# Performance work log

Measured on AMD Instinct MI355X. Metric: run time of the kernel, lower is better.

Reference implementation:

```python
import jax, jax.numpy as jnp
import numpy as np

HEADS = 64
DIM_HEAD = 64
SCALE = DIM_HEAD ** -0.5
EPS = 1e-6


def setup_inputs() -> dict:
    key = jax.random.key(0)
    ks = jax.random.split(key, 6)
    b, s, dim = 2, 4096, 1024
    inner = HEADS * DIM_HEAD  # 4096
    std = 0.02
    return {
        "x": jax.random.normal(ks[0], (b, s, dim), dtype=jnp.float32),
        "Wq": jax.random.normal(ks[1], (dim, inner), dtype=jnp.float32) * std,
        "Wk": jax.random.normal(ks[2], (dim, inner), dtype=jnp.float32) * std,
        "Wv": jax.random.normal(ks[3], (dim, inner), dtype=jnp.float32) * std,
        "Wo": jax.random.normal(ks[4], (inner, dim), dtype=jnp.float32) * std,
        "bo": jnp.zeros((dim,), dtype=jnp.float32),
    }


def reference(x, Wq, Wk, Wv, Wo, bo):
    b, s, dim = x.shape
    h, dh = HEADS, DIM_HEAD
    # projections -> [b, s, h, dh]
    q = (x @ Wq).reshape(b, s, h, dh)
    k = (x @ Wk).reshape(b, s, h, dh)
    v = (x @ Wv).reshape(b, s, h, dh)
    # kernel feature map (relu) + scale on q
    q = jax.nn.relu(q) * SCALE
    k = jax.nn.relu(k)
    # NOTE: faithful to the source, these einsums contract over the HEAD axis
    # per token (i, j index heads; d indexes dim_head).
    kv = jnp.einsum('bsid,bsjd->bsdj', k, v)          # [b, s, dh, h]
    out = jnp.einsum('bsid,bsdj->bsij', q, kv)        # [b, s, h, h]
    q_norm = jnp.einsum('bsid,bsd->bsi', q, k.sum(axis=2))  # [b, s, h]
    out = out / (q_norm[..., None] + EPS)
    out = out.reshape(b, s, h * h)                    # h*h == h*dh since h == dh
    return out @ Wo + bo
```

## Files before the change

### kernel.cpp

```cpp
#include <hip/hip_runtime.h>
#include <hip/hip_bf16.h>
#include <cstdint>

#define M_TOK 8192
#define DIM   1024
#define INNER 4096
#define HEADS 64
#define DH    64
#define QSCALE 0.125f
#define EPS    1e-6f

typedef __hip_bfloat16 bf16;
typedef __bf16 bf16x8_t __attribute__((ext_vector_type(8)));
typedef float f32x4_t __attribute__((ext_vector_type(4)));

__device__ __forceinline__ float bfbits2f(unsigned short u) {
  return __uint_as_float(((unsigned)u) << 16);
}
__device__ __forceinline__ unsigned short f2bfbits(float f) {
  __hip_bfloat16 h = __float2bfloat16(f);
  unsigned short u;
  __builtin_memcpy(&u, &h, 2);
  return u;
}

__device__ __forceinline__ void load_lds16(const void* g, void* l) {
  __builtin_amdgcn_global_load_lds(
      (__attribute__((address_space(1))) void*)g,
      (__attribute__((address_space(3))) void*)l, 16, 0, 0);
}

__device__ __forceinline__ void asm_barrier() {
  asm volatile("s_barrier" ::: "memory");
}

#define LGKM_SB(N) do { \
    asm volatile("s_waitcnt lgkmcnt(" #N ")" ::: "memory"); \
    __builtin_amdgcn_sched_barrier(0); } while (0)

__device__ __forceinline__ void swizzle_xy(int& bx, int& by) {
  const int gx = gridDim.x, gy = gridDim.y;
  const int id  = blockIdx.x + gx * blockIdx.y;
  const int per = gy >> 3;
  const int xcd = id & 7;
  const int s   = id >> 3;
  by = xcd * per + (s % per);
  bx = s / per;
}

__global__ __launch_bounds__(256) void prep_kernel(
    const float* __restrict__ x, unsigned short* __restrict__ xb,
    const float* __restrict__ Wk, const float* __restrict__ Wv,
    unsigned short* __restrict__ WtKV)
{
  const int bid = blockIdx.x;
  if (bid < 8192) {
    const int i = bid * 256 + threadIdx.x;
    const float4 v = reinterpret_cast<const float4*>(x)[i];
    ushort4 o;
    o.x = f2bfbits(v.x); o.y = f2bfbits(v.y);
    o.z = f2bfbits(v.z); o.w = f2bfbits(v.w);
    reinterpret_cast<ushort4*>(xb)[i] = o;
    return;
  }
  __shared__ float tile[32][33];
  const int t    = bid - 8192;
  const int z    = t >> 12;
  const int tt   = t & 4095;
  const float* W = z ? Wv : Wk;
  unsigned short* dst = WtKV + (size_t)z * DIM * INNER;
  const int bx = (tt & 127) * 32;
  const int by = (tt >> 7) * 32;
  const int tx = threadIdx.x & 31;
  const int ty = threadIdx.x >> 5;
#pragma unroll
  for (int k = 0; k < 4; ++k)
    tile[ty + k * 8][tx] = W[(size_t)(by + ty + k * 8) * INNER + bx + tx];
  __syncthreads();
#pragma unroll
  for (int k = 0; k < 4; ++k)
    dst[(size_t)(bx + ty + k * 8) * DIM + by + tx] = f2bfbits(tile[tx][ty + k * 8]);
}

__global__ __launch_bounds__(256) void tcast_kernel(
    const float* __restrict__ W, unsigned short* __restrict__ Wt, int R, int C)
{
  __shared__ float tile[32][33];
  const int bx = blockIdx.x * 32;
  const int by = blockIdx.y * 32;
  const int tx = threadIdx.x & 31;
  const int ty = threadIdx.x >> 5;
#pragma unroll
  for (int k = 0; k < 4; ++k)
    tile[ty + k * 8][tx] = W[(size_t)(by + ty + k * 8) * C + bx + tx];
  __syncthreads();
#pragma unroll
  for (int k = 0; k < 4; ++k)
    Wt[(size_t)(bx + ty + k * 8) * R + by + tx] = f2bfbits(tile[tx][ty + k * 8]);
}

__device__ __forceinline__ void stage_half(
    const unsigned short* __restrict__ G, unsigned short* L,
    int rowbase, int k0, int K, int h, int tid)
{
#pragma unroll
  for (int j = 0; j < 2; ++j) {
    const int q  = h * 1024 + j * 512 + tid;
    const int r  = q >> 3;
    const int cg = (tid & 7) ^ (r & 7);
    load_lds16(&G[(size_t)(rowbase + r) * K + k0 + cg * 8], &L[q * 8]);
  }
}

__device__ __forceinline__ void read_af4(
    const unsigned short* __restrict__ Ac, bf16x8_t (&af)[8][2],
    int m0, int wm, int l15, int quad)
{
#pragma unroll
  for (int mt = 0; mt < 4; ++mt) {
    const int r = wm + (m0 + mt) * 16 + l15;
#pragma unroll
    for (int kt = 0; kt < 2; ++kt) {
      const int s = (kt * 4 + quad) ^ (r & 7);
      af[m0 + mt][kt] = *reinterpret_cast<const bf16x8_t*>(&Ac[r * 64 + s * 8]);
    }
  }
}

__device__ __forceinline__ void read_bf2(
    const unsigned short* __restrict__ Bc, bf16x8_t (&bfr)[4][2],
    int n0, int wn, int l15, int quad)
{
#pragma unroll
  for (int nt = 0; nt < 2; ++nt) {
    const int r = wn + (n0 + nt) * 16 + l15;
#pragma unroll
    for (int kt = 0; kt < 2; ++kt) {
      const int s = (kt * 4 + quad) ^ (r & 7);
      bfr[n0 + nt][kt] = *reinterpret_cast<const bf16x8_t*>(&Bc[r * 64 + s * 8]);
    }
  }
}

__device__ __forceinline__ void mfma_quad(
    f32x4_t (&acc)[8][4], const bf16x8_t (&af)[8][2],
    const bf16x8_t (&bfr)[4][2], int m0, int n0)
{
  __builtin_amdgcn_s_setprio(1);
#pragma unroll
  for (int mt = m0; mt < m0 + 4; ++mt)
#pragma unroll
    for (int nt = n0; nt < n0 + 2; ++nt) {
      acc[mt][nt] = __builtin_amdgcn_mfma_f32_16x16x32_bf16(
          af[mt][0], bfr[nt][0], acc[mt][nt], 0, 0, 0);
      acc[mt][nt] = __builtin_amdgcn_mfma_f32_16x16x32_bf16(
          af[mt][1], bfr[nt][1], acc[mt][nt], 0, 0, 0);
    }
  __builtin_amdgcn_s_setprio(0);
}

template <int MODE, int DUAL>
__global__ __launch_bounds__(512, 2) void gemm256(
    const unsigned short* __restrict__ A,
    const unsigned short* __restrict__ Bt,
    unsigned short* __restrict__ C0,
    unsigned short* __restrict__ C1,
    int N, int K)
{
  __shared__ __align__(16) unsigned short As[2][256 * 64];
  __shared__ __align__(16) unsigned short Bs[2][256 * 64];

  int bxi, byi;
  swizzle_xy(bxi, byi);
  const int tid  = threadIdx.x;
  const int bm   = byi * 256;
  const int bn   = bxi * 256;
  const int lane = tid & 63;
  const int w    = tid >> 6;
  const int wm   = (w >> 2) * 128;
  const int wn   = (w & 3) * 64;
  const int quad = lane >> 4;
  const int l15  = lane & 15;

  f32x4_t acc[8][4];
#pragma unroll
  for (int mt = 0; mt < 8; ++mt)
#pragma unroll
    for (int nt = 0; nt < 4; ++nt) acc[mt][nt] = (f32x4_t){0.f, 0.f, 0.f, 0.f};

  const int NT = K >> 6;

  bf16x8_t af[8][2], bfr[4][2];

  stage_half(A,  As[0], bm, 0,  K, 0, tid);
  stage_half(A,  As[0], bm, 0,  K, 1, tid);
  stage_half(Bt, Bs[0], bn, 0,  K, 0, tid);
  stage_half(Bt, Bs[0], bn, 0,  K, 1, tid);
  stage_half(A,  As[1], bm, 64, K, 0, tid);
  stage_half(A,  As[1], bm, 64, K, 1, tid);
  asm volatile("s_waitcnt vmcnt(4)" ::: "memory");
  asm_barrier();
  __builtin_amdgcn_sched_barrier(0);
  read_af4(As[0], af, 0, wm, l15, quad);
  read_bf2(Bs[0], bfr, 0, wn, l15, quad);

  for (int T = 0; T < NT; ++T) {
    const int c = T & 1;
    const unsigned short* Ac = As[c];
    const unsigned short* Bc = Bs[c];
    unsigned short* Bnx = Bs[c ^ 1];
    unsigned short* Anx = As[c];
    const int kB = (T + 1) * 64;
    const int kA = (T + 2) * 64;
    const bool pB = (T + 1 < NT);
    const bool pA = (T + 2 < NT);

    read_af4(Ac, af, 4, wm, l15, quad);
    LGKM_SB(8);
    mfma_quad(acc, af, bfr, 0, 0);

    read_bf2(Bc, bfr, 2, wn, l15, quad);
    if (pB) stage_half(Bt, Bnx, bn, kB, K, 0, tid);
    LGKM_SB(4);
    mfma_quad(acc, af, bfr, 4, 0);

    if (pB) stage_half(Bt, Bnx, bn, kB, K, 1, tid);
    if (pA) stage_half(A, Anx, bm, kA, K, 0, tid);
    LGKM_SB(0);
    mfma_quad(acc, af, bfr, 0, 2);

    if (pA) stage_half(A, Anx, bm, kA, K, 1, tid);
    mfma_quad(acc, af, bfr, 4, 2);
    if (T < NT - 2) {
      asm volatile("s_waitcnt vmcnt(4)" ::: "memory");
    } else {
      asm volatile("s_waitcnt vmcnt(0)" ::: "memory");
    }
    asm_barrier();
    __builtin_amdgcn_sched_barrier(0);
    if (T + 1 < NT) {
      read_af4(As[c ^ 1], af, 0, wm, l15, quad);
      read_bf2(Bs[c ^ 1], bfr, 0, wn, l15, quad);
    }
  }

  if (DUAL) {
    const bool isK = (bn < 4096);
    unsigned short* __restrict__ C = isK ? C0 : C1;
    const int bnc = bn & 4095;
#pragma unroll
    for (int mt = 0; mt < 8; ++mt)
#pragma unroll
      for (int i = 0; i < 4; ++i) {
        const size_t rowg = (size_t)(bm + wm + mt * 16 + quad * 4 + i);
#pragma unroll
        for (int nt = 0; nt < 4; ++nt) {
          float v = acc[mt][nt][i];
          if (isK) v = fmaxf(v, 0.f);
          C[rowg * 4096 + bnc + wn + nt * 16 + l15] = f2bfbits(v);
        }
      }
  } else {
#pragma unroll
    for (int mt = 0; mt < 8; ++mt)
#pragma unroll
      for (int i = 0; i < 4; ++i) {
        const size_t rowg = (size_t)(bm + wm + mt * 16 + quad * 4 + i);
#pragma unroll
        for (int nt = 0; nt < 4; ++nt) {
          float v = acc[mt][nt][i];
          if (MODE >= 1) v = fmaxf(v, 0.f);
          if (MODE == 2) v *= QSCALE;
          C0[rowg * (size_t)N + bn + wn + nt * 16 + l15] = f2bfbits(v);
        }
      }
  }
}

__global__ __launch_bounds__(256) void gemm_out_bf16(
    const unsigned short* __restrict__ A,
    const unsigned short* __restrict__ Bt,
    const float* __restrict__ bias,
    float* __restrict__ out, int M, int N, int K)
{
  __shared__ __align__(16) unsigned short As[128 * 64];
  __shared__ __align__(16) unsigned short Bs[64 * 64];

  int bxi, byi;
  swizzle_xy(bxi, byi);
  const int tid  = threadIdx.x;
  const int bm   = byi * 128;
  const int bn   = bxi * 64;
  const int lane = tid & 63;
  const int w    = tid >> 6;
  const int wm   = (w & 1) * 64;
  const int wn   = (w >> 1) * 32;
  const int quad = lane >> 4;
  const int l15  = lane & 15;

  f32x4_t acc[4][2];
#pragma unroll
  for (int mt = 0; mt < 4; ++mt)
#pragma unroll
    for (int nt = 0; nt < 2; ++nt) acc[mt][nt] = (f32x4_t){0.f, 0.f, 0.f, 0.f};

  int qa[4], ra[4], ca[4];
#pragma unroll
  for (int j = 0; j < 4; ++j) {
    qa[j] = tid + 256 * j;
    ra[j] = qa[j] >> 3;
    ca[j] = (qa[j] & 7) ^ (ra[j] & 7);
  }
  int qb[2], rb[2], cb[2];
#pragma unroll
  for (int j = 0; j < 2; ++j) {
    qb[j] = tid + 256 * j;
    rb[j] = qb[j] >> 3;
    cb[j] = (qb[j] & 7) ^ (rb[j] & 7);
  }

  for (int k0 = 0; k0 < K; k0 += 64) {
    __syncthreads();
#pragma unroll
    for (int j = 0; j < 4; ++j)
      load_lds16(&A[(size_t)(bm + ra[j]) * K + k0 + ca[j] * 8], &As[qa[j] * 8]);
#pragma unroll
    for (int j = 0; j < 2; ++j)
      load_lds16(&Bt[(size_t)(bn + rb[j]) * K + k0 + cb[j] * 8], &Bs[qb[j] * 8]);
    __syncthreads();

    bf16x8_t af[4][2], bfr[2][2];
#pragma unroll
    for (int mt = 0; mt < 4; ++mt) {
      const int r = wm + mt * 16 + l15;
#pragma unroll
      for (int kt = 0; kt < 2; ++kt) {
        const int slot = (kt * 4 + quad) ^ (r & 7);
        af[mt][kt] = *reinterpret_cast<const bf16x8_t*>(&As[r * 64 + slot * 8]);
      }
    }
#pragma unroll
    for (int nt = 0; nt < 2; ++nt) {
      const int r = wn + nt * 16 + l15;
#pragma unroll
      for (int kt = 0; kt < 2; ++kt) {
        const int slot = (kt * 4 + quad) ^ (r & 7);
        bfr[nt][kt] = *reinterpret_cast<const bf16x8_t*>(&Bs[r * 64 + slot * 8]);
      }
    }
#pragma unroll
    for (int mt = 0; mt < 4; ++mt)
#pragma unroll
      for (int nt = 0; nt < 2; ++nt) {
        acc[mt][nt] = __builtin_amdgcn_mfma_f32_16x16x32_bf16(
            af[mt][0], bfr[nt][0], acc[mt][nt], 0, 0, 0);
        acc[mt][nt] = __builtin_amdgcn_mfma_f32_16x16x32_bf16(
            af[mt][1], bfr[nt][1], acc[mt][nt], 0, 0, 0);
      }
  }

#pragma unroll
  for (int mt = 0; mt < 4; ++mt)
#pragma unroll
    for (int i = 0; i < 4; ++i) {
      const size_t rowg = (size_t)(bm + wm + mt * 16 + quad * 4 + i);
#pragma unroll
      for (int nt = 0; nt < 2; ++nt) {
        const int colg = bn + wn + nt * 16 + l15;
        out[rowg * N + colg] = acc[mt][nt][i] + bias[colg];
      }
    }
}

__global__ __launch_bounds__(256) void ksum_kernel(
    const unsigned short* __restrict__ Kb, float* __restrict__ ks)
{
  const int t = blockIdx.x * 4 + (threadIdx.x >> 6);
  const int j = threadIdx.x & 63;
  const uint4* row = reinterpret_cast<const uint4*>(Kb + (size_t)t * INNER);
  float s[8] = {0.f, 0.f, 0.f, 0.f, 0.f, 0.f, 0.f, 0.f};
#pragma unroll
  for (int m = 0; m < 8; ++m) {
    const uint4 u = row[j + 64 * m];
    s[0] += __uint_as_float((u.x & 0xFFFFu) << 16);
    s[1] += __uint_as_float(u.x & 0xFFFF0000u);
    s[2] += __uint_as_float((u.y & 0xFFFFu) << 16);
    s[3] += __uint_as_float(u.y & 0xFFFF0000u);
    s[4] += __uint_as_float((u.z & 0xFFFFu) << 16);
    s[5] += __uint_as_float(u.z & 0xFFFF0000u);
    s[6] += __uint_as_float((u.w & 0xFFFFu) << 16);
    s[7] += __uint_as_float(u.w & 0xFFFF0000u);
  }
#pragma unroll
  for (int off = 8; off < 64; off <<= 1)
#pragma unroll
    for (int e = 0; e < 8; ++e) s[e] += __shfl_xor(s[e], off, 64);
  if (j < 8) {
    float4* dst = reinterpret_cast<float4*>(ks + t * 64 + j * 8);
    float4 lo, hi;
    lo.x = s[0]; lo.y = s[1]; lo.z = s[2]; lo.w = s[3];
    hi.x = s[4]; hi.y = s[5]; hi.z = s[6]; hi.w = s[7];
    dst[0] = lo; dst[1] = hi;
  }
}

__global__ __launch_bounds__(256) void attn_mfma(
    const unsigned short* __restrict__ Qb, const unsigned short* __restrict__ Vb,
    const float* __restrict__ ksum, unsigned short* __restrict__ Ab)
{
  const int t    = blockIdx.x * 4 + (threadIdx.x >> 6);
  const int lane = threadIdx.x & 63;
  const int l15  = lane & 15;
  const int quad = lane >> 4;
  const size_t base = (size_t)t * INNER;

  union VU { bf16x8_t v; unsigned short u[8]; };

  float ksv[2][8];
#pragma unroll
  for (int kt = 0; kt < 2; ++kt) {
    const float4* p = reinterpret_cast<const float4*>(ksum + t * 64 + kt * 32 + quad * 8);
    const float4 a = p[0], b = p[1];
    ksv[kt][0] = a.x; ksv[kt][1] = a.y; ksv[kt][2] = a.z; ksv[kt][3] = a.w;
    ksv[kt][4] = b.x; ksv[kt][5] = b.y; ksv[kt][6] = b.z; ksv[kt][7] = b.w;
  }

  bf16x8_t vs[4][2];
#pragma unroll
  for (int nt = 0; nt < 4; ++nt)
#pragma unroll
    for (int kt = 0; kt < 2; ++kt) {
      VU vr, vo;
      vr.v = *reinterpret_cast<const bf16x8_t*>(
          Vb + base + (size_t)(nt * 16 + l15) * 64 + kt * 32 + quad * 8);
#pragma unroll
      for (int j = 0; j < 8; ++j)
        vo.u[j] = f2bfbits(bfbits2f(vr.u[j]) * ksv[kt][j]);
      vs[nt][kt] = vo.v;
    }

  bf16x8_t qf[4][2];
  float qn[4] = {0.f, 0.f, 0.f, 0.f};
#pragma unroll
  for (int mt = 0; mt < 4; ++mt)
#pragma unroll
    for (int kt = 0; kt < 2; ++kt) {
      VU qr;
      qr.v = *reinterpret_cast<const bf16x8_t*>(
          Qb + base + (size_t)(mt * 16 + l15) * 64 + kt * 32 + quad * 8);
      qf[mt][kt] = qr.v;
#pragma unroll
      for (int j = 0; j < 8; ++j)
        qn[mt] += bfbits2f(qr.u[j]) * ksv[kt][j];
    }
#pragma unroll
  for (int mt = 0; mt < 4; ++mt) {
    qn[mt] += __shfl_xor(qn[mt], 16, 64);
    qn[mt] += __shfl_xor(qn[mt], 32, 64);
  }

  f32x4_t acc[4][4];
#pragma unroll
  for (int mt = 0; mt < 4; ++mt)
#pragma unroll
    for (int nt = 0; nt < 4; ++nt) acc[mt][nt] = (f32x4_t){0.f, 0.f, 0.f, 0.f};

#pragma unroll
  for (int mt = 0; mt < 4; ++mt)
#pragma unroll
    for (int nt = 0; nt < 4; ++nt) {
      acc[mt][nt] = __builtin_amdgcn_mfma_f32_16x16x32_bf16(
          qf[mt][0], vs[nt][0], acc[mt][nt], 0, 0, 0);
      acc[mt][nt] = __builtin_amdgcn_mfma_f32_16x16x32_bf16(
          qf[mt][1], vs[nt][1], acc[mt][nt], 0, 0, 0);
    }

#pragma unroll
  for (int mt = 0; mt < 4; ++mt)
#pragma unroll
    for (int i = 0; i < 4; ++i) {
      const float inv = 1.f / (__shfl(qn[mt], quad * 4 + i, 64) + EPS);
      const size_t roff = base + (size_t)(mt * 16 + quad * 4 + i) * 64;
#pragma unroll
      for (int nt = 0; nt < 4; ++nt)
        Ab[roff + nt * 16 + l15] = f2bfbits(acc[mt][nt][i] * inv);
    }
}

extern "C" void kernel_launch(void* const* d_in, const int* in_sizes, int n_in,
                              void* d_out, int out_size, void* d_ws, size_t ws_size,
                              hipStream_t stream)
{
  const float* x  = (const float*)d_in[0];
  const float* Wq = (const float*)d_in[1];
  const float* Wk = (const float*)d_in[2];
  const float* Wv = (const float*)d_in[3];
  const float* Wo = (const float*)d_in[4];
  const float* bo = (const float*)d_in[5];
  float* out = (float*)d_out;

  uint8_t* ws = (uint8_t*)d_ws;
  const size_t HALF = (size_t)M_TOK * INNER * sizeof(bf16);
  unsigned short* KQA = (unsigned short*)ws;
  unsigned short* Vb  = (unsigned short*)(ws + HALF);
  float* ks           = (float*)(ws + 2 * HALF);

  unsigned short* Xb   = (unsigned short*)d_out;
  unsigned short* WtKV = (unsigned short*)((uint8_t*)d_out + (16u << 20));
  unsigned short* WqT  = WtKV;
  unsigned short* Wot  = Vb;

  const dim3 blk(256);
  const dim3 blk512(512);

  prep_kernel<<<dim3(16384), blk, 0, stream>>>(x, Xb, Wk, Wv, WtKV);

  gemm256<0, 1><<<dim3(2 * INNER / 256, M_TOK / 256), blk512, 0, stream>>>(
      Xb, WtKV, KQA, Vb, 2 * INNER, DIM);

  ksum_kernel<<<dim3(M_TOK / 4), blk, 0, stream>>>(KQA, ks);

  tcast_kernel<<<dim3(INNER / 32, DIM / 32), blk, 0, stream>>>(
      Wq, WqT, DIM, INNER);

  gemm256<2, 0><<<dim3(INNER / 256, M_TOK / 256), blk512, 0, stream>>>(
      Xb, WqT, KQA, nullptr, INNER, DIM);

  attn_mfma<<<dim3(M_TOK / 4), blk, 0, stream>>>(KQA, Vb, ks, KQA);

  tcast_kernel<<<dim3(DIM / 32, INNER / 32), blk, 0, stream>>>(
      Wo, Wot, INNER, DIM);

  gemm_out_bf16<<<dim3(DIM / 64, M_TOK / 128), blk, 0, stream>>>(
      KQA, Wot, bo, out, M_TOK, DIM, INNER);
}
```

Before: 484.8 us.

## Fuse K head-sum into KV projection GEMM epilogue via permuted Wk columns

```diff
diff --git a/kernel.cpp b/kernel.cpp
--- a/kernel.cpp
+++ b/kernel.cpp
@@ -78,8 +78,11 @@
     tile[ty + k * 8][tx] = W[(size_t)(by + ty + k * 8) * INNER + bx + tx];
   __syncthreads();
 #pragma unroll
-  for (int k = 0; k < 4; ++k)
-    dst[(size_t)(bx + ty + k * 8) * DIM + by + tx] = f2bfbits(tile[tx][ty + k * 8]);
+  for (int k = 0; k < 4; ++k) {
+    const int c  = bx + ty + k * 8;
+    const int rp = z ? c : (((c & 63) << 6) | (c >> 6));
+    dst[(size_t)rp * DIM + by + tx] = f2bfbits(tile[tx][ty + k * 8]);
+  }
 }
 
 __global__ __launch_bounds__(256) void tcast_kernel(
@@ -165,6 +168,7 @@
     const unsigned short* __restrict__ Bt,
     unsigned short* __restrict__ C0,
     unsigned short* __restrict__ C1,
+    float* __restrict__ ks,
     int N, int K)
 {
   __shared__ __align__(16) unsigned short As[2][256 * 64];
@@ -245,21 +249,36 @@
   }
 
   if (DUAL) {
-    const bool isK = (bn < 4096);
-    unsigned short* __restrict__ C = isK ? C0 : C1;
-    const int bnc = bn & 4095;
-#pragma unroll
-    for (int mt = 0; mt < 8; ++mt)
-#pragma unroll
-      for (int i = 0; i < 4; ++i) {
-        const size_t rowg = (size_t)(bm + wm + mt * 16 + quad * 4 + i);
-#pragma unroll
-        for (int nt = 0; nt < 4; ++nt) {
-          float v = acc[mt][nt][i];
-          if (isK) v = fmaxf(v, 0.f);
-          C[rowg * 4096 + bnc + wn + nt * 16 + l15] = f2bfbits(v);
+    if (bn < 4096) {
+      const int dh = (bn + wn) >> 6;
+#pragma unroll
+      for (int mt = 0; mt < 8; ++mt)
+#pragma unroll
+        for (int i = 0; i < 4; ++i) {
+          float s = 0.f;
+#pragma unroll
+          for (int nt = 0; nt < 4; ++nt) s += fmaxf(acc[mt][nt][i], 0.f);
+          s += __shfl_xor(s, 1, 16);
+          s += __shfl_xor(s, 2, 16);
+          s += __shfl_xor(s, 4, 16);
+          s += __shfl_xor(s, 8, 16);
+          if (l15 == 0) {
+            const size_t rowg = (size_t)(bm + wm + mt * 16 + quad * 4 + i);
+            ks[rowg * 64 + dh] = s;
+          }
         }
-      }
+    } else {
+      const int bnc = bn & 4095;
+#pragma unroll
+      for (int mt = 0; mt < 8; ++mt)
+#pragma unroll
+        for (int i = 0; i < 4; ++i) {
+          const size_t rowg = (size_t)(bm + wm + mt * 16 + quad * 4 + i);
+#pragma unroll
+          for (int nt = 0; nt < 4; ++nt)
+            C1[rowg * 4096 + bnc + wn + nt * 16 + l15] = f2bfbits(acc[mt][nt][i]);
+        }
+    }
   } else {
 #pragma unroll
     for (int mt = 0; mt < 8; ++mt)
@@ -372,38 +391,6 @@
     }
 }
 
-__global__ __launch_bounds__(256) void ksum_kernel(
-    const unsigned short* __restrict__ Kb, float* __restrict__ ks)
-{
-  const int t = blockIdx.x * 4 + (threadIdx.x >> 6);
-  const int j = threadIdx.x & 63;
-  const uint4* row = reinterpret_cast<const uint4*>(Kb + (size_t)t * INNER);
-  float s[8] = {0.f, 0.f, 0.f, 0.f, 0.f, 0.f, 0.f, 0.f};
-#pragma unroll
-  for (int m = 0; m < 8; ++m) {
-    const uint4 u = row[j + 64 * m];
-    s[0] += __uint_as_float((u.x & 0xFFFFu) << 16);
-    s[1] += __uint_as_float(u.x & 0xFFFF0000u);
-    s[2] += __uint_as_float((u.y & 0xFFFFu) << 16);
-    s[3] += __uint_as_float(u.y & 0xFFFF0000u);
-    s[4] += __uint_as_float((u.z & 0xFFFFu) << 16);
-    s[5] += __uint_as_float(u.z & 0xFFFF0000u);
-    s[6] += __uint_as_float((u.w & 0xFFFFu) << 16);
-    s[7] += __uint_as_float(u.w & 0xFFFF0000u);
-  }
-#pragma unroll
-  for (int off = 8; off < 64; off <<= 1)
-#pragma unroll
-    for (int e = 0; e < 8; ++e) s[e] += __shfl_xor(s[e], off, 64);
-  if (j < 8) {
-    float4* dst = reinterpret_cast<float4*>(ks + t * 64 + j * 8);
-    float4 lo, hi;
-    lo.x = s[0]; lo.y = s[1]; lo.z = s[2]; lo.w = s[3];
-    hi.x = s[4]; hi.y = s[5]; hi.z = s[6]; hi.w = s[7];
-    dst[0] = lo; dst[1] = hi;
-  }
-}
-
 __global__ __launch_bounds__(256) void attn_mfma(
     const unsigned short* __restrict__ Qb, const unsigned short* __restrict__ Vb,
     const float* __restrict__ ksum, unsigned short* __restrict__ Ab)
@@ -516,15 +503,13 @@
   prep_kernel<<<dim3(16384), blk, 0, stream>>>(x, Xb, Wk, Wv, WtKV);
 
   gemm256<0, 1><<<dim3(2 * INNER / 256, M_TOK / 256), blk512, 0, stream>>>(
-      Xb, WtKV, KQA, Vb, 2 * INNER, DIM);
-
-  ksum_kernel<<<dim3(M_TOK / 4), blk, 0, stream>>>(KQA, ks);
+      Xb, WtKV, nullptr, Vb, ks, 2 * INNER, DIM);
 
   tcast_kernel<<<dim3(INNER / 32, DIM / 32), blk, 0, stream>>>(
       Wq, WqT, DIM, INNER);
 
   gemm256<2, 0><<<dim3(INNER / 256, M_TOK / 256), blk512, 0, stream>>>(
-      Xb, WqT, KQA, nullptr, INNER, DIM);
+      Xb, WqT, KQA, nullptr, nullptr, INNER, DIM);
 
   attn_mfma<<<dim3(M_TOK / 4), blk, 0, stream>>>(KQA, Vb, ks, KQA);
 
```

Measured after the change: 453.9 us. -6.4%, faster.
